# Optimization experiments

Hardware: AMD Instinct MI355X
Metric: run time of the kernel (lower is better)

The kernel has to match this reference:

```python
import jax, jax.numpy as jnp
import numpy as np
from jax import lax

B, T, D, H, Z, L = 64, 1024, 128, 512, 64, 2

def lstm_layer(x_tbd, h0, c0, Wih, Whh, bih, bhh):
    # x_tbd: [T,B,Din]; precompute input contribution (big GEMM outside scan)
    gx = jnp.einsum('tbd,gd->tbg', x_tbd, Wih) + (bih + bhh)  # [T,B,4H]
    def step(carry, gxt):
        h, c = carry
        gates = gxt + h @ Whh.T
        i, f, g, o = jnp.split(gates, 4, axis=-1)
        c = jax.nn.sigmoid(f) * c + jax.nn.sigmoid(i) * jnp.tanh(g)
        h = jax.nn.sigmoid(o) * jnp.tanh(c)
        return (h, c), h
    (hT, cT), hs = lax.scan(step, (h0, c0), gx)
    return hs, hT, cT  # hs: [T,B,H]

def run_lstm(x_btd, h0_l, c0_l, params):
    # params: list of (Wih, Whh, bih, bhh) per layer; h0_l/c0_l: [L,B,H]
    seq = jnp.transpose(x_btd, (1, 0, 2))
    hTs = []
    for l, (Wih, Whh, bih, bhh) in enumerate(params):
        seq, hT, cT = lstm_layer(seq, h0_l[l], c0_l[l], Wih, Whh, bih, bhh)
        hTs.append(hT)
    return jnp.transpose(seq, (1, 0, 2)), jnp.stack(hTs)

def setup_inputs() -> dict:
    key = jax.random.key(0)
    ks = iter(jax.random.split(key, 32))
    s = 0.05
    d = {'x': jax.random.uniform(next(ks), (B, T, D), jnp.float32)}
    for pre in ('enc', 'dec'):
        for l in range(L):
            din = D if l == 0 else H
            d[f'{pre}_Wih{l}'] = jax.random.normal(next(ks), (4 * H, din), jnp.float32) * s
            d[f'{pre}_Whh{l}'] = jax.random.normal(next(ks), (4 * H, H), jnp.float32) * s
            d[f'{pre}_bih{l}'] = jnp.zeros((4 * H,), jnp.float32)
            d[f'{pre}_bhh{l}'] = jnp.zeros((4 * H,), jnp.float32)
    d['tl_W'] = jax.random.normal(next(ks), (Z, H), jnp.float32) * s
    d['tl_b'] = jnp.zeros((Z,), jnp.float32)
    d['lh_W'] = jax.random.normal(next(ks), (H * L, Z), jnp.float32) * s
    d['lh_b'] = jnp.zeros((H * L,), jnp.float32)
    d['op_W'] = jax.random.normal(next(ks), (D, H), jnp.float32) * s
    d['op_b'] = jnp.zeros((D,), jnp.float32)
    return d

def reference(x, enc_Wih0, enc_Whh0, enc_bih0, enc_bhh0, enc_Wih1, enc_Whh1, enc_bih1, enc_bhh1,
              dec_Wih0, dec_Whh0, dec_bih0, dec_bhh0, dec_Wih1, dec_Whh1, dec_bih1, dec_bhh1,
              tl_W, tl_b, lh_W, lh_b, op_W, op_b):
    enc_p = [(enc_Wih0, enc_Whh0, enc_bih0, enc_bhh0), (enc_Wih1, enc_Whh1, enc_bih1, enc_bhh1)]
    dec_p = [(dec_Wih0, dec_Whh0, dec_bih0, dec_bhh0), (dec_Wih1, dec_Whh1, dec_bih1, dec_bhh1)]
    zeros_lbh = jnp.zeros((L, B, H), x.dtype)
    # encode
    _, h_n = run_lstm(x, zeros_lbh, zeros_lbh, enc_p)
    z = h_n[-1] @ tl_W.T + tl_b  # [B,Z]
    # decode: zero input sequence, latent-derived initial hidden state
    init_h = jnp.tanh(z @ lh_W.T + lh_b).reshape(B, L, H).transpose(1, 0, 2)  # matches torch .view(L,B,H)? no
    init_h = jnp.tanh(z @ lh_W.T + lh_b).reshape(L, B, H)  # torch: view(num_layers, batch, hidden) on [B, H*L] flat -- faithful to source
    dec_in = jnp.zeros((B, T, D), x.dtype)
    dec_out, _ = run_lstm(dec_in, init_h, jnp.zeros_like(init_h), dec_p)
    recon = jax.nn.sigmoid(jnp.einsum('bth,dh->btd', dec_out, op_W) + op_b)
    return recon, z
```

## Files before the change

kernel.cpp:

```cpp
#include <hip/hip_runtime.h>
#include <cstdint>
#include <cstddef>

typedef unsigned short u16;
typedef unsigned int u32;
typedef __attribute__((ext_vector_type(8))) short short8;
typedef __attribute__((ext_vector_type(4))) float f32x4;

#define AGENT_SCOPE __HIP_MEMORY_SCOPE_AGENT
#define SPIN_CAP 20000000
#define POLL_CAP 200000
#define SENT 0xFFFFFFFFu

__device__ __forceinline__ u16 f2bf(float f) {
  u32 u = __float_as_uint(f);
  return (u16)((u + 0x7FFFu + ((u >> 16) & 1u)) >> 16);
}
__device__ __forceinline__ float bf2f(u16 s) { return __uint_as_float(((u32)s) << 16); }
__device__ __forceinline__ float sigm(float x) { return 1.f / (1.f + __expf(-x)); }
__device__ __forceinline__ float tanha(float x) { return 1.f - 2.f / (__expf(2.f * x) + 1.f); }
__device__ __forceinline__ void wait_vm0() { asm volatile("s_waitcnt vmcnt(0)" ::: "memory"); }

__global__ void __launch_bounds__(256, 1)
lstm_ae_kernel(const float* __restrict__ x,
    const float* __restrict__ eWih0, const float* __restrict__ eWhh0,
    const float* __restrict__ ebi0,  const float* __restrict__ ebh0,
    const float* __restrict__ eWih1, const float* __restrict__ eWhh1,
    const float* __restrict__ ebi1,  const float* __restrict__ ebh1,
    const float* __restrict__ dWhh0,
    const float* __restrict__ dbi0,  const float* __restrict__ dbh0,
    const float* __restrict__ dWih1, const float* __restrict__ dWhh1,
    const float* __restrict__ dbi1,  const float* __restrict__ dbh1,
    const float* __restrict__ tlW,   const float* __restrict__ tlb,
    const float* __restrict__ lhW,   const float* __restrict__ lhb,
    const float* __restrict__ opW,   const float* __restrict__ opb,
    float* __restrict__ out, char* __restrict__ wsb)
{
  __shared__ __align__(16) u16 sH0[16 * 520];
  __shared__ __align__(16) u16 sH1[16 * 520];
  __shared__ __align__(16) u16 sX[16 * 136];
  __shared__ __align__(16) u16 sOPW[2 * 520];
  __shared__ float sP[4 * 256];
  __shared__ float sBias[64];
  __shared__ float sC[256];
  __shared__ float sZ[16 * 64];
  __shared__ float sOPB[4];

  u32* gcnt  = (u32*)wsb;
  float* zbuf= (float*)(wsb + 4096);
  u32* h0r   = (u32*)(wsb + 32768);
  u32* h1r   = (u32*)(wsb + 229376);

  const int tid  = threadIdx.x;
  const int col  = blockIdx.x & 3;
  const int rowg = blockIdx.x >> 2;
  const int wid  = tid >> 6;
  const int lane = tid & 63;
  const int m    = lane & 15;
  const int qo   = (lane >> 4) * 8;

  auto stage_slot = [&](int q0, int q1, bool p0on, bool p1on) {
    const u32* b0 = h0r + ((q0 * 4 + col) << 12) + tid;
    const u32* b1 = h1r + ((q1 * 4 + col) << 12) + tid;
    u32 v0[16], v1[16];
    int it = 0; bool ok = false;
    while (!ok && it++ < POLL_CAP) {
      ok = true;
      if (p0on) {
        #pragma unroll
        for (int i = 0; i < 16; ++i) {
          v0[i] = __hip_atomic_load(b0 + i * 256, __ATOMIC_RELAXED, AGENT_SCOPE);
          ok &= (v0[i] != SENT);
        }
      }
      if (p1on) {
        #pragma unroll
        for (int i = 0; i < 16; ++i) {
          v1[i] = __hip_atomic_load(b1 + i * 256, __ATOMIC_RELAXED, AGENT_SCOPE);
          ok &= (v1[i] != SENT);
        }
      }
    }
    u32* dH0 = (u32*)sH0; u32* dH1 = (u32*)sH1;
    #pragma unroll
    for (int i = 0; i < 16; ++i) {
      int g = i * 256 + tid;
      int rg = g >> 6, b = (g >> 2) & 15, udw = g & 3;
      if (p0on) dH0[b * 260 + rg * 4 + udw] = v0[i];
      if (p1on) dH1[b * 260 + rg * 4 + udw] = v1[i];
    }
  };

  auto clears = [&](int s) {
    if (tid < 64) {
      int cq0 = (s + 1) % 3, cq1 = s % 3;
      __hip_atomic_store(h0r + ((cq0 * 4 + col) << 12) + (rowg << 6) + tid,
                         SENT, __ATOMIC_RELAXED, AGENT_SCOPE);
      __hip_atomic_store(h1r + ((cq1 * 4 + col) << 12) + (rowg << 6) + tid,
                         SENT, __ATOMIC_RELAXED, AGENT_SCOPE);
    }
  };

  auto stage_xt = [&](int s) {
    int b = tid >> 4, seg = tid & 15;
    const float* p = x + (size_t)(col * 16 + b) * 131072 + (size_t)s * 128 + seg * 8;
    float4 f0 = *(const float4*)p, f1 = *(const float4*)(p + 4);
    uint4 v;
    v.x = (u32)f2bf(f0.x) | ((u32)f2bf(f0.y) << 16);
    v.y = (u32)f2bf(f0.z) | ((u32)f2bf(f0.w) << 16);
    v.z = (u32)f2bf(f1.x) | ((u32)f2bf(f1.y) << 16);
    v.w = (u32)f2bf(f1.z) | ((u32)f2bf(f1.w) << 16);
    *(uint4*)(sX + b * 136 + seg * 8) = v;
  };

  auto ldw = [&](const float* W, int ld, int row, int kofs) -> short8 {
    const float* p = W + (size_t)row * ld + kofs + qo;
    float4 f0 = *(const float4*)p, f1 = *(const float4*)(p + 4);
    short8 r;
    r[0] = (short)f2bf(f0.x); r[1] = (short)f2bf(f0.y);
    r[2] = (short)f2bf(f0.z); r[3] = (short)f2bf(f0.w);
    r[4] = (short)f2bf(f1.x); r[5] = (short)f2bf(f1.y);
    r[6] = (short)f2bf(f1.z); r[7] = (short)f2bf(f1.w);
    return r;
  };

  auto act_store = [&](bool L0a, bool L1a, int q0, int q1) {
    int li = tid >> 7, b = (tid >> 3) & 15, u = tid & 7;
    bool actv = li ? L1a : L0a;
    float hv = 0.f;
    if (actv) {
      float gi = sP[(li*2)*256   + b*16 + u]     + sBias[li*32 + u];
      float gf = sP[(li*2)*256   + b*16 + 8 + u] + sBias[li*32 + 8 + u];
      float gg = sP[(li*2+1)*256 + b*16 + u]     + sBias[li*32 + 16 + u];
      float go = sP[(li*2+1)*256 + b*16 + 8 + u] + sBias[li*32 + 24 + u];
      float c = sC[(li*16 + b)*8 + u];
      c = sigm(gf)*c + sigm(gi)*tanha(gg);
      sC[(li*16 + b)*8 + u] = c;
      hv = sigm(go)*tanha(c);
    }
    u16 hb = f2bf(hv);
    u32 other = __shfl_xor((u32)hb, 1);
    if (actv && !(u & 1)) {
      u32 v = (u32)hb | (other << 16);
      u32* ring = li ? h1r : h0r;
      int q = li ? q1 : q0;
      __hip_atomic_store(ring + ((q * 4 + col) << 12) + (rowg << 6) + b * 4 + (u >> 1),
                         v, __ATOMIC_RELAXED, AGENT_SCOPE);
    }
  };

  auto gbar = [&](u32 target) {
    __syncthreads();
    if (tid == 0) {
      __hip_atomic_fetch_add(gcnt, 1u, __ATOMIC_RELEASE, AGENT_SCOPE);
      int it = 0;
      while (__hip_atomic_load(gcnt, __ATOMIC_RELAXED, AGENT_SCOPE) < target && ++it < SPIN_CAP) {}
      (void)__hip_atomic_load(gcnt, __ATOMIC_ACQUIRE, AGENT_SCOPE);
    }
    __syncthreads();
  };

  const int nl = (wid & 1) * 16 + m;
  const int gw = ((nl >> 3) << 9) + rowg * 8 + (nl & 7);

  short8 wb[32];

  if (wid < 2) {
    #pragma unroll
    for (int t = 0; t < 4; ++t)  wb[t]      = ldw(eWih0, 128, gw, t * 32);
    #pragma unroll
    for (int t = 0; t < 16; ++t) wb[4 + t]  = ldw(eWhh0, 512, gw, t * 32);
  } else {
    #pragma unroll
    for (int t = 0; t < 16; ++t) wb[t]      = ldw(eWih1, 512, gw, t * 32);
    #pragma unroll
    for (int t = 0; t < 16; ++t) wb[16 + t] = ldw(eWhh1, 512, gw, t * 32);
  }
  if (tid < 64) {
    int li = tid >> 5, n = tid & 31;
    int g = ((n >> 3) << 9) + rowg * 8 + (n & 7);
    sBias[li * 32 + n] = li ? (ebi1[g] + ebh1[g]) : (ebi0[g] + ebh0[g]);
  }
  sC[tid] = 0.f;
  __syncthreads();

  for (int s = 0; s <= 1024; ++s) {
    const bool L0 = (s < 1024), L1 = (s >= 1);
    if (L0) stage_xt(s);
    stage_slot((s + 2) % 3, (s + 1) % 3, true, s >= 1);
    __syncthreads();
    clears(s);

    f32x4 acc = {0.f, 0.f, 0.f, 0.f};
    if (wid < 2) {
      if (L0) {
        #pragma unroll
        for (int t = 0; t < 4; ++t) {
          short8 a = *(const short8*)(sX + m * 136 + t * 32 + qo);
          acc = __builtin_amdgcn_mfma_f32_16x16x32_bf16(a, wb[t], acc, 0, 0, 0);
        }
        #pragma unroll
        for (int t = 0; t < 16; ++t) {
          short8 a = *(const short8*)(sH0 + m * 520 + t * 32 + qo);
          acc = __builtin_amdgcn_mfma_f32_16x16x32_bf16(a, wb[4 + t], acc, 0, 0, 0);
        }
      }
    } else {
      if (L1) {
        #pragma unroll
        for (int t = 0; t < 16; ++t) {
          short8 a = *(const short8*)(sH0 + m * 520 + t * 32 + qo);
          acc = __builtin_amdgcn_mfma_f32_16x16x32_bf16(a, wb[t], acc, 0, 0, 0);
        }
        #pragma unroll
        for (int t = 0; t < 16; ++t) {
          short8 a = *(const short8*)(sH1 + m * 520 + t * 32 + qo);
          acc = __builtin_amdgcn_mfma_f32_16x16x32_bf16(a, wb[16 + t], acc, 0, 0, 0);
        }
      }
    }
    {
      bool wact = (wid < 2) ? L0 : L1;
      if (wact) {
        int mb = (lane >> 4) * 4;
        #pragma unroll
        for (int r = 0; r < 4; ++r) sP[wid * 256 + (mb + r) * 16 + m] = acc[r];
      }
    }
    __syncthreads();
    act_store(L0, L1, s % 3, (s + 2) % 3);
  }

  {
    const u32* b1 = h1r + ((0 * 4 + col) << 12) + tid;
    u32 v1[16];
    int it = 0; bool ok = false;
    while (!ok && it++ < POLL_CAP) {
      ok = true;
      #pragma unroll
      for (int i = 0; i < 16; ++i) {
        v1[i] = __hip_atomic_load(b1 + i * 256, __ATOMIC_RELAXED, AGENT_SCOPE);
        ok &= (v1[i] != SENT);
      }
    }
    u32* dH1 = (u32*)sH1;
    #pragma unroll
    for (int i = 0; i < 16; ++i) {
      int g = i * 256 + tid;
      dH1[((g >> 2) & 15) * 260 + (g >> 6) * 4 + (g & 3)] = v1[i];
    }
  }
  __syncthreads();
  if (tid < 16) {
    int b = tid;
    float acc = tlb[rowg];
    for (int kk = 0; kk < 512; kk += 8) {
      short8 hv = *(const short8*)(sH1 + b * 520 + kk);
      #pragma unroll
      for (int j = 0; j < 8; ++j) acc += bf2f((u16)hv[j]) * tlW[rowg * 512 + kk + j];
    }
    int gb = col * 16 + b;
    __hip_atomic_store((u32*)zbuf + gb * 64 + rowg, __float_as_uint(acc),
                       __ATOMIC_RELAXED, AGENT_SCOPE);
    out[8388608 + gb * 64 + rowg] = acc;
  }
  gbar(256);

  if (tid < 64) {
    #pragma unroll
    for (int q = 0; q < 3; ++q) {
      __hip_atomic_store(h0r + ((q * 4 + col) << 12) + (rowg << 6) + tid,
                         SENT, __ATOMIC_RELAXED, AGENT_SCOPE);
      __hip_atomic_store(h1r + ((q * 4 + col) << 12) + (rowg << 6) + tid,
                         SENT, __ATOMIC_RELAXED, AGENT_SCOPE);
    }
  }
  wait_vm0();

  if (wid < 2) {
    #pragma unroll
    for (int t = 0; t < 16; ++t) wb[t] = ldw(dWhh0, 512, gw, t * 32);
  } else {
    #pragma unroll
    for (int t = 0; t < 16; ++t) wb[t]      = ldw(dWih1, 512, gw, t * 32);
    #pragma unroll
    for (int t = 0; t < 16; ++t) wb[16 + t] = ldw(dWhh1, 512, gw, t * 32);
  }
  if (tid < 64) {
    int li = tid >> 5, n = tid & 31;
    int g = ((n >> 3) << 9) + rowg * 8 + (n & 7);
    sBias[li * 32 + n] = li ? (dbi1[g] + dbh1[g]) : (dbi0[g] + dbh0[g]);
  }
  for (int i = tid; i < 2 * 64; i += 256) {
    int dd = i >> 6, k = (i & 63) * 8;
    const float* p = opW + (size_t)(rowg * 2 + dd) * 512 + k;
    float4 f0 = *(const float4*)p, f1 = *(const float4*)(p + 4);
    uint4 v;
    v.x = (u32)f2bf(f0.x) | ((u32)f2bf(f0.y) << 16);
    v.y = (u32)f2bf(f0.z) | ((u32)f2bf(f0.w) << 16);
    v.z = (u32)f2bf(f1.x) | ((u32)f2bf(f1.y) << 16);
    v.w = (u32)f2bf(f1.z) | ((u32)f2bf(f1.w) << 16);
    *(uint4*)(sOPW + dd * 520 + k) = v;
  }
  if (tid < 2) sOPB[tid] = opb[rowg * 2 + tid];
  sC[tid] = 0.f;

  {
    int ri = tid >> 4, kk = (tid & 15) * 4;
    int zr = ((ri >> 3) << 5) + 8 * col + (ri & 7);
    #pragma unroll
    for (int j = 0; j < 4; ++j)
      sZ[ri * 64 + kk + j] = __uint_as_float(
          __hip_atomic_load((u32*)zbuf + zr * 64 + kk + j, __ATOMIC_RELAXED, AGENT_SCOPE));
  }
  __syncthreads();
  {
    int li = tid >> 7, hh = (tid >> 4) & 7, qb = (tid >> 3) & 1, u = tid & 7;
    int cc = qb * 512 + rowg * 8 + u;
    int bl = 2 * hh + qb;
    float acc2 = lhb[cc];
    const float* lw = lhW + (size_t)cc * 64;
    #pragma unroll 8
    for (int k = 0; k < 64; ++k) acc2 += sZ[(li * 8 + hh) * 64 + k] * lw[k];
    u16 hb = f2bf(tanha(acc2));
    u32 other = __shfl_xor((u32)hb, 1);
    if (!(u & 1)) {
      u32 v = (u32)hb | (other << 16);
      u32* ring = li ? h1r : h0r;
      __hip_atomic_store(ring + ((2 * 4 + col) << 12) + (rowg << 6) + bl * 4 + (u >> 1),
                         v, __ATOMIC_RELAXED, AGENT_SCOPE);
    }
  }
  gbar(512);

  for (int s = 0; s <= 1025; ++s) {
    const bool L0 = (s < 1024), L1 = (s >= 1 && s <= 1024), RC = (s >= 2);
    stage_slot((s + 2) % 3, (s + 1) % 3, s <= 1024, s >= 1);
    __syncthreads();
    clears(s);

    f32x4 acc = {0.f, 0.f, 0.f, 0.f};
    if (wid < 2) {
      if (L0) {
        #pragma unroll
        for (int t = 0; t < 16; ++t) {
          short8 a = *(const short8*)(sH0 + m * 520 + t * 32 + qo);
          acc = __builtin_amdgcn_mfma_f32_16x16x32_bf16(a, wb[t], acc, 0, 0, 0);
        }
      }
    } else {
      if (L1) {
        #pragma unroll
        for (int t = 0; t < 16; ++t) {
          short8 a = *(const short8*)(sH0 + m * 520 + t * 32 + qo);
          acc = __builtin_amdgcn_mfma_f32_16x16x32_bf16(a, wb[t], acc, 0, 0, 0);
        }
        #pragma unroll
        for (int t = 0; t < 16; ++t) {
          short8 a = *(const short8*)(sH1 + m * 520 + t * 32 + qo);
          acc = __builtin_amdgcn_mfma_f32_16x16x32_bf16(a, wb[16 + t], acc, 0, 0, 0);
        }
      }
    }
    {
      bool wact = (wid < 2) ? L0 : L1;
      if (wact) {
        int mb = (lane >> 4) * 4;
        #pragma unroll
        for (int r = 0; r < 4; ++r) sP[wid * 256 + (mb + r) * 16 + m] = acc[r];
      }
    }
    __syncthreads();
    act_store(L0, L1, s % 3, (s + 2) % 3);

    if (RC) {
      __syncthreads();
      int b = tid >> 4, dd = (tid >> 3) & 1, pt = tid & 7;
      float acc2 = 0.f;
      int k0 = pt * 64;
      for (int kk = 0; kk < 64; kk += 8) {
        short8 hv = *(const short8*)(sH1 + b * 520 + k0 + kk);
        short8 wv = *(const short8*)(sOPW + dd * 520 + k0 + kk);
        #pragma unroll
        for (int j = 0; j < 8; ++j) acc2 += bf2f((u16)hv[j]) * bf2f((u16)wv[j]);
      }
      sP[tid] = acc2;
      __syncthreads();
      if (tid < 32) {
        int b2 = tid >> 1, d2 = tid & 1;
        float sum = sOPB[d2];
        #pragma unroll
        for (int j = 0; j < 8; ++j) sum += sP[b2 * 16 + d2 * 8 + j];
        out[(size_t)(col * 16 + b2) * 131072 + (size_t)(s - 2) * 128 + rowg * 2 + d2]
            = sigm(sum);
      }
    }
  }
}

extern "C" void kernel_launch(void* const* d_in, const int* in_sizes, int n_in,
                              void* d_out, int out_size, void* d_ws, size_t ws_size,
                              hipStream_t stream) {
  (void)in_sizes; (void)n_in; (void)out_size; (void)ws_size;
  char* ws = (char*)d_ws;
  hipMemsetAsync(ws, 0, 32768, stream);
  hipMemsetAsync(ws + 32768, 0xFF, 131072, stream);
  hipMemsetAsync(ws + 163840, 0x00, 65536, stream);
  hipMemsetAsync(ws + 229376, 0xFF, 131072, stream);
  hipMemsetAsync(ws + 360448, 0x00, 65536, stream);
  lstm_ae_kernel<<<dim3(256), dim3(256), 0, stream>>>(
      (const float*)d_in[0],
      (const float*)d_in[1],  (const float*)d_in[2],
      (const float*)d_in[3],  (const float*)d_in[4],
      (const float*)d_in[5],  (const float*)d_in[6],
      (const float*)d_in[7],  (const float*)d_in[8],
      (const float*)d_in[10],
      (const float*)d_in[11], (const float*)d_in[12],
      (const float*)d_in[13], (const float*)d_in[14],
      (const float*)d_in[15], (const float*)d_in[16],
      (const float*)d_in[17], (const float*)d_in[18],
      (const float*)d_in[19], (const float*)d_in[20],
      (const float*)d_in[21], (const float*)d_in[22],
      (float*)d_out, (char*)d_ws);
}
```

Baseline: 6.334 ms.

## Compute decoder output projection with MFMA in wave 0 and prefetch x loads

```diff
diff --git a/kernel.cpp b/kernel.cpp
--- a/kernel.cpp
+++ b/kernel.cpp
@@ -39,7 +39,6 @@
   __shared__ __align__(16) u16 sH0[16 * 520];
   __shared__ __align__(16) u16 sH1[16 * 520];
   __shared__ __align__(16) u16 sX[16 * 136];
-  __shared__ __align__(16) u16 sOPW[2 * 520];
   __shared__ float sP[4 * 256];
   __shared__ float sBias[64];
   __shared__ float sC[256];
@@ -99,18 +98,6 @@
       __hip_atomic_store(h1r + ((cq1 * 4 + col) << 12) + (rowg << 6) + tid,
                          SENT, __ATOMIC_RELAXED, AGENT_SCOPE);
     }
-  };
-
-  auto stage_xt = [&](int s) {
-    int b = tid >> 4, seg = tid & 15;
-    const float* p = x + (size_t)(col * 16 + b) * 131072 + (size_t)s * 128 + seg * 8;
-    float4 f0 = *(const float4*)p, f1 = *(const float4*)(p + 4);
-    uint4 v;
-    v.x = (u32)f2bf(f0.x) | ((u32)f2bf(f0.y) << 16);
-    v.y = (u32)f2bf(f0.z) | ((u32)f2bf(f0.w) << 16);
-    v.z = (u32)f2bf(f1.x) | ((u32)f2bf(f1.y) << 16);
-    v.w = (u32)f2bf(f1.z) | ((u32)f2bf(f1.w) << 16);
-    *(uint4*)(sX + b * 136 + seg * 8) = v;
   };
 
   auto ldw = [&](const float* W, int ld, int row, int kofs) -> short8 {
@@ -186,8 +173,21 @@
 
   for (int s = 0; s <= 1024; ++s) {
     const bool L0 = (s < 1024), L1 = (s >= 1);
-    if (L0) stage_xt(s);
+    float4 xf0, xf1;
+    const int xb = tid >> 4, xseg = tid & 15;
+    if (L0) {
+      const float* p = x + (size_t)(col * 16 + xb) * 131072 + (size_t)s * 128 + xseg * 8;
+      xf0 = *(const float4*)p; xf1 = *(const float4*)(p + 4);
+    }
     stage_slot((s + 2) % 3, (s + 1) % 3, true, s >= 1);
+    if (L0) {
+      uint4 v;
+      v.x = (u32)f2bf(xf0.x) | ((u32)f2bf(xf0.y) << 16);
+      v.y = (u32)f2bf(xf0.z) | ((u32)f2bf(xf0.w) << 16);
+      v.z = (u32)f2bf(xf1.x) | ((u32)f2bf(xf1.y) << 16);
+      v.w = (u32)f2bf(xf1.z) | ((u32)f2bf(xf1.w) << 16);
+      *(uint4*)(sX + xb * 136 + xseg * 8) = v;
+    }
     __syncthreads();
     clears(s);
 
@@ -277,9 +277,19 @@
   }
   wait_vm0();
 
+  short8 rcw[16];
+  {
+    const short8 rz = {0, 0, 0, 0, 0, 0, 0, 0};
+    #pragma unroll
+    for (int t = 0; t < 16; ++t) rcw[t] = rz;
+  }
   if (wid < 2) {
     #pragma unroll
     for (int t = 0; t < 16; ++t) wb[t] = ldw(dWhh0, 512, gw, t * 32);
+    if (wid == 0 && nl < 2) {
+      #pragma unroll
+      for (int t = 0; t < 16; ++t) rcw[t] = ldw(opW, 512, rowg * 2 + nl, t * 32);
+    }
   } else {
     #pragma unroll
     for (int t = 0; t < 16; ++t) wb[t]      = ldw(dWih1, 512, gw, t * 32);
@@ -290,17 +300,6 @@
     int li = tid >> 5, n = tid & 31;
     int g = ((n >> 3) << 9) + rowg * 8 + (n & 7);
     sBias[li * 32 + n] = li ? (dbi1[g] + dbh1[g]) : (dbi0[g] + dbh0[g]);
-  }
-  for (int i = tid; i < 2 * 64; i += 256) {
-    int dd = i >> 6, k = (i & 63) * 8;
-    const float* p = opW + (size_t)(rowg * 2 + dd) * 512 + k;
-    float4 f0 = *(const float4*)p, f1 = *(const float4*)(p + 4);
-    uint4 v;
-    v.x = (u32)f2bf(f0.x) | ((u32)f2bf(f0.y) << 16);
-    v.y = (u32)f2bf(f0.z) | ((u32)f2bf(f0.w) << 16);
-    v.z = (u32)f2bf(f1.x) | ((u32)f2bf(f1.y) << 16);
-    v.w = (u32)f2bf(f1.z) | ((u32)f2bf(f1.w) << 16);
-    *(uint4*)(sOPW + dd * 520 + k) = v;
   }
   if (tid < 2) sOPB[tid] = opb[rowg * 2 + tid];
   sC[tid] = 0.f;
@@ -339,7 +338,8 @@
     __syncthreads();
     clears(s);
 
-    f32x4 acc = {0.f, 0.f, 0.f, 0.f};
+    f32x4 acc  = {0.f, 0.f, 0.f, 0.f};
+    f32x4 racc = {0.f, 0.f, 0.f, 0.f};
     if (wid < 2) {
       if (L0) {
         #pragma unroll
@@ -360,6 +360,13 @@
           short8 a = *(const short8*)(sH1 + m * 520 + t * 32 + qo);
           acc = __builtin_amdgcn_mfma_f32_16x16x32_bf16(a, wb[16 + t], acc, 0, 0, 0);
         }
+      }
+    }
+    if (wid == 0 && RC) {
+      #pragma unroll
+      for (int t = 0; t < 16; ++t) {
+        short8 a = *(const short8*)(sH1 + m * 520 + t * 32 + qo);
+        racc = __builtin_amdgcn_mfma_f32_16x16x32_bf16(a, rcw[t], racc, 0, 0, 0);
       }
     }
     {
@@ -372,27 +379,12 @@
     }
     __syncthreads();
     act_store(L0, L1, s % 3, (s + 2) % 3);
-
-    if (RC) {
-      __syncthreads();
-      int b = tid >> 4, dd = (tid >> 3) & 1, pt = tid & 7;
-      float acc2 = 0.f;
-      int k0 = pt * 64;
-      for (int kk = 0; kk < 64; kk += 8) {
-        short8 hv = *(const short8*)(sH1 + b * 520 + k0 + kk);
-        short8 wv = *(const short8*)(sOPW + dd * 520 + k0 + kk);
-        #pragma unroll
-        for (int j = 0; j < 8; ++j) acc2 += bf2f((u16)hv[j]) * bf2f((u16)wv[j]);
-      }
-      sP[tid] = acc2;
-      __syncthreads();
-      if (tid < 32) {
-        int b2 = tid >> 1, d2 = tid & 1;
-        float sum = sOPB[d2];
-        #pragma unroll
-        for (int j = 0; j < 8; ++j) sum += sP[b2 * 16 + d2 * 8 + j];
-        out[(size_t)(col * 16 + b2) * 131072 + (size_t)(s - 2) * 128 + rowg * 2 + d2]
-            = sigm(sum);
+    if (wid == 0 && RC && m < 2) {
+      #pragma unroll
+      for (int r = 0; r < 4; ++r) {
+        int b = (lane >> 4) * 4 + r;
+        out[(size_t)(col * 16 + b) * 131072 + (size_t)(s - 2) * 128 + rowg * 2 + m]
+            = sigm(racc[r] + sOPB[m]);
       }
     }
   }
```

Result: slower. 6.561 ms (+3.6%).
